# Performance work log

Hardware: AMD Instinct MI355X
Metric: run time of the kernel (lower is better)

The kernel has to match this reference:

```python
import jax, jax.numpy as jnp
import numpy as np


def setup_inputs() -> dict:
    key = jax.random.key(0)
    k1, k2, k3 = jax.random.split(key, 3)
    B, H, L, OUT = 4096, 2048, 8, 1024
    x = jax.random.normal(k1, (B, H), dtype=jnp.float32)
    W = jax.random.normal(k2, (L, H, H), dtype=jnp.float32)
    beta = jax.random.normal(k3, (H, OUT), dtype=jnp.float32)
    return {"x": x, "W": W, "beta": beta}


def _fcn_forward(x, W, beta):
    h = W.shape[-1]
    scale = 1.0 / jnp.sqrt(jnp.asarray(h, x.dtype))
    # Linear1d: (x[:,None]*W).sum(-1)/sqrt(h) == x @ W.T / sqrt(h); then ReLU.
    def layer(y, Wi):
        y = jax.nn.relu(jnp.einsum('bi,oi->bo', y, Wi) * scale)
        return y, None
    y, _ = jax.lax.scan(layer, x, W)
    # readout: y @ beta / h
    return jnp.einsum('bh,ho->bo', y, beta) / h


def reference(x, W, beta):
    return _fcn_forward(x, W, beta)
```

## Files before the change

kernel.cpp:

```cpp
#include <hip/hip_runtime.h>
#include <cstdint>
#include <cstddef>

typedef __bf16          bf16x8  __attribute__((ext_vector_type(8)));
typedef float           f32x4   __attribute__((ext_vector_type(4)));
typedef unsigned short  u16x8   __attribute__((ext_vector_type(8)));

__device__ __forceinline__ unsigned short f32_bf16_rne(float f) {
  union { float f; unsigned u; } v; v.f = f;
  unsigned u = v.u + 0x7FFFu + ((v.u >> 16) & 1u);
  return (unsigned short)(u >> 16);
}

__global__ void cvt_f32_bf16(const float* __restrict__ in,
                             unsigned short* __restrict__ out, int n8) {
  int idx = blockIdx.x * 256 + threadIdx.x;
  int stride = gridDim.x * 256;
  for (int i = idx; i < n8; i += stride) {
    float4 a = ((const float4*)in)[2 * (size_t)i];
    float4 b = ((const float4*)in)[2 * (size_t)i + 1];
    u16x8 o;
    o[0] = f32_bf16_rne(a.x); o[1] = f32_bf16_rne(a.y);
    o[2] = f32_bf16_rne(a.z); o[3] = f32_bf16_rne(a.w);
    o[4] = f32_bf16_rne(b.x); o[5] = f32_bf16_rne(b.y);
    o[6] = f32_bf16_rne(b.z); o[7] = f32_bf16_rne(b.w);
    *(u16x8*)(out + (size_t)i * 8) = o;
  }
}

__global__ void cvt_transpose(const float* __restrict__ in,
                              unsigned short* __restrict__ out, int H, int O) {
  __shared__ float tile[32][33];
  int o0 = blockIdx.x * 32, h0 = blockIdx.y * 32;
  int tx = threadIdx.x & 31, ty = threadIdx.x >> 5;
  #pragma unroll
  for (int i = ty; i < 32; i += 8)
    tile[i][tx] = in[(size_t)(h0 + i) * O + (o0 + tx)];
  __syncthreads();
  #pragma unroll
  for (int i = ty; i < 32; i += 8)
    out[(size_t)(o0 + i) * H + (h0 + tx)] = f32_bf16_rne(tile[tx][i]);
}

#define GLOAD(gp, lp)                                                   \
  __builtin_amdgcn_global_load_lds(                                     \
      (const __attribute__((address_space(1))) void*)(gp),              \
      (__attribute__((address_space(3))) void*)(lp), 16, 0, 0)

#define MFMA16 __builtin_amdgcn_mfma_f32_16x16x32_bf16


#define PHASE(KK, STAGE)                                                      \
  do {                                                                        \
    const int c = cc##KK;                                                     \
    bf16x8 a0 = *(const bf16x8*)(cA + aBase + 0 * 1024 + c);                  \
    bf16x8 a1 = *(const bf16x8*)(cA + aBase + 1 * 1024 + c);                  \
    bf16x8 a2 = *(const bf16x8*)(cA + aBase + 2 * 1024 + c);                  \
    bf16x8 a3 = *(const bf16x8*)(cA + aBase + 3 * 1024 + c);                  \
    bf16x8 b0 = *(const bf16x8*)(cB + bBase + 0 * 1024 + c);                  \
    bf16x8 b1 = *(const bf16x8*)(cB + bBase + 1 * 1024 + c);                  \
    bf16x8 b2 = *(const bf16x8*)(cB + bBase + 2 * 1024 + c);                  \
    bf16x8 b3 = *(const bf16x8*)(cB + bBase + 3 * 1024 + c);                  \
    STAGE                                                                     \
    __builtin_amdgcn_sched_barrier(0);                                        \
    __builtin_amdgcn_s_barrier();                                             \
    asm volatile("s_waitcnt lgkmcnt(0)" ::: "memory");                        \
    __builtin_amdgcn_sched_barrier(0);                                        \
    __builtin_amdgcn_s_setprio(1);                                            \
    acc[0][0] = MFMA16(a0, b0, acc[0][0], 0, 0, 0);                           \
    acc[0][1] = MFMA16(a0, b1, acc[0][1], 0, 0, 0);                           \
    acc[0][2] = MFMA16(a0, b2, acc[0][2], 0, 0, 0);                           \
    acc[0][3] = MFMA16(a0, b3, acc[0][3], 0, 0, 0);                           \
    acc[1][0] = MFMA16(a1, b0, acc[1][0], 0, 0, 0);                           \
    acc[1][1] = MFMA16(a1, b1, acc[1][1], 0, 0, 0);                           \
    acc[1][2] = MFMA16(a1, b2, acc[1][2], 0, 0, 0);                           \
    acc[1][3] = MFMA16(a1, b3, acc[1][3], 0, 0, 0);                           \
    acc[2][0] = MFMA16(a2, b0, acc[2][0], 0, 0, 0);                           \
    acc[2][1] = MFMA16(a2, b1, acc[2][1], 0, 0, 0);                           \
    acc[2][2] = MFMA16(a2, b2, acc[2][2], 0, 0, 0);                           \
    acc[2][3] = MFMA16(a2, b3, acc[2][3], 0, 0, 0);                           \
    acc[3][0] = MFMA16(a3, b0, acc[3][0], 0, 0, 0);                           \
    acc[3][1] = MFMA16(a3, b1, acc[3][1], 0, 0, 0);                           \
    acc[3][2] = MFMA16(a3, b2, acc[3][2], 0, 0, 0);                           \
    acc[3][3] = MFMA16(a3, b3, acc[3][3], 0, 0, 0);                           \
    __builtin_amdgcn_s_setprio(0);                                            \
    __builtin_amdgcn_sched_barrier(0);                                        \
    __builtin_amdgcn_s_barrier();                                             \
  } while (0)

__global__ __launch_bounds__(512, 2)
void gemm128x256(const unsigned short* __restrict__ A,
                 const unsigned short* __restrict__ B,
                 unsigned short* __restrict__ Cp, int N, int K, float scale) {
  __shared__ __bf16 As[3 * 128 * 64] __attribute__((aligned(16)));
  __shared__ __bf16 Bs[3 * 256 * 64] __attribute__((aligned(16)));

  const int tid  = threadIdx.x;
  const int lane = tid & 63;
  const int wave = tid >> 6;
  const int wr   = wave >> 2;
  const int wc   = wave & 3;
  const int l16  = lane & 15;
  const int kgrp = lane >> 4;

  const int brow0 = blockIdx.y * 128;
  const int bcol0 = blockIdx.x * 256;

  const int xorv  = (l16 & 7) << 3;
  const int cc0   = (kgrp * 8) ^ xorv;
  const int cc1   = (32 + kgrp * 8) ^ xorv;
  const int aBase = (wr * 64 + l16) * 64;
  const int bBase = (wc * 64 + l16) * 64;

  const int srow = tid >> 3;
  const int scol = ((tid & 7) * 8) ^ ((srow & 7) << 3);
  const unsigned short* gA0 = A + (size_t)(brow0 +   0 + srow) * K + scol;
  const unsigned short* gA1 = A + (size_t)(brow0 +  64 + srow) * K + scol;
  const unsigned short* gB0 = B + (size_t)(bcol0 +   0 + srow) * K + scol;
  const unsigned short* gB1 = B + (size_t)(bcol0 +  64 + srow) * K + scol;
  const unsigned short* gB2 = B + (size_t)(bcol0 + 128 + srow) * K + scol;
  const unsigned short* gB3 = B + (size_t)(bcol0 + 192 + srow) * K + scol;

  f32x4 acc[4][4] = {};

  const int NT = K >> 6;

  {
    GLOAD(gA0, &As[0 * 4096 + tid * 8]);
    GLOAD(gA1, &As[1 * 4096 + tid * 8]);
    GLOAD(gB0, &Bs[0 * 4096 + tid * 8]);
    GLOAD(gB1, &Bs[1 * 4096 + tid * 8]);
    GLOAD(gB2, &Bs[2 * 4096 + tid * 8]);
    GLOAD(gB3, &Bs[3 * 4096 + tid * 8]);
    GLOAD(gA0 + 64, &As[8192 + 0 * 4096 + tid * 8]);
    GLOAD(gA1 + 64, &As[8192 + 1 * 4096 + tid * 8]);
    GLOAD(gB0 + 64, &Bs[16384 + 0 * 4096 + tid * 8]);
    GLOAD(gB1 + 64, &Bs[16384 + 1 * 4096 + tid * 8]);
    GLOAD(gB2 + 64, &Bs[16384 + 2 * 4096 + tid * 8]);
    GLOAD(gB3 + 64, &Bs[16384 + 3 * 4096 + tid * 8]);
    asm volatile("s_waitcnt vmcnt(6)" ::: "memory");
    __builtin_amdgcn_s_barrier();
  }

  int s = 0;
  for (int t = 0; t < NT; ++t) {
    const __bf16* cA = &As[s * 8192];
    const __bf16* cB = &Bs[s * 16384];
    int su = s + 2; if (su >= 3) su -= 3;
    __bf16* dA = &As[su * 8192];
    __bf16* dB = &Bs[su * 16384];
    const bool stg = (t < NT - 2);
    const size_t ko = (size_t)(t + 2) * 64;

    PHASE(0,
      if (stg) {
        GLOAD(gA0 + ko, dA + 0 * 4096 + tid * 8);
        GLOAD(gA1 + ko, dA + 1 * 4096 + tid * 8);
        GLOAD(gB0 + ko, dB + 0 * 4096 + tid * 8);
      }
    );
    PHASE(1,
      if (stg) {
        GLOAD(gB1 + ko, dB + 1 * 4096 + tid * 8);
        GLOAD(gB2 + ko, dB + 2 * 4096 + tid * 8);
        GLOAD(gB3 + ko, dB + 3 * 4096 + tid * 8);
        asm volatile("s_waitcnt vmcnt(6)" ::: "memory");
      } else if (t == NT - 2) {
        asm volatile("s_waitcnt vmcnt(0)" ::: "memory");
      }
    );
    s = s + 1; if (s == 3) s = 0;
  }

  const int crow0 = brow0 + wr * 64 + kgrp * 4;
  const int ccol0 = bcol0 + wc * 64 + l16;
  #pragma unroll
  for (int m = 0; m < 4; ++m)
    #pragma unroll
    for (int n = 0; n < 4; ++n)
      #pragma unroll
      for (int j = 0; j < 4; ++j) {
        float v = acc[m][n][j] * scale;
        v = v > 0.0f ? v : 0.0f;
        Cp[(size_t)(crow0 + m * 16 + j) * N + (ccol0 + n * 16)] = f32_bf16_rne(v);
      }
}

__global__ __launch_bounds__(256)
void gemm_bt_f32(const unsigned short* __restrict__ A,
                 const unsigned short* __restrict__ B,
                 float* __restrict__ C, int N, int K, float scale) {
  __shared__ __bf16 As[128 * 32] __attribute__((aligned(16)));
  __shared__ __bf16 Bs[128 * 32] __attribute__((aligned(16)));

  const int tid  = threadIdx.x;
  const int lane = tid & 63;
  const int wave = tid >> 6;
  const int wr   = wave >> 1, wc = wave & 1;
  const int l16  = lane & 15, kgrp = lane >> 4;

  const int brow0 = blockIdx.y * 128;
  const int bcol0 = blockIdx.x * 128;

  const int offb  = wave * 2048 + lane * 16;
  const int srow  = offb >> 6;
  const int selem = (offb & 63) >> 1;
  const unsigned short* gA0 = A + (size_t)(brow0 + srow) * K + selem;
  const unsigned short* gA1 = A + (size_t)(brow0 + srow + 16) * K + selem;
  const unsigned short* gB0 = B + (size_t)(bcol0 + srow) * K + selem;
  const unsigned short* gB1 = B + (size_t)(bcol0 + srow + 16) * K + selem;
  __bf16* lA0 = &As[wave * 1024];
  __bf16* lA1 = &As[wave * 1024 + 512];
  __bf16* lB0 = &Bs[wave * 1024];
  __bf16* lB1 = &Bs[wave * 1024 + 512];

  f32x4 acc[4][4] = {};
  const int aoff = (wr * 64 + l16) * 32 + kgrp * 8;
  const int boff = (wc * 64 + l16) * 32 + kgrp * 8;

  for (int k0 = 0; k0 < K; k0 += 32) {
    GLOAD(gA0 + k0, lA0);
    GLOAD(gA1 + k0, lA1);
    GLOAD(gB0 + k0, lB0);
    GLOAD(gB1 + k0, lB1);
    asm volatile("s_waitcnt vmcnt(0)" ::: "memory");
    __syncthreads();

    bf16x8 af[4], bfv[4];
    #pragma unroll
    for (int m = 0; m < 4; ++m)
      af[m] = *(const bf16x8*)(As + aoff + m * 16 * 32);
    #pragma unroll
    for (int n = 0; n < 4; ++n)
      bfv[n] = *(const bf16x8*)(Bs + boff + n * 16 * 32);
    #pragma unroll
    for (int m = 0; m < 4; ++m)
      #pragma unroll
      for (int n = 0; n < 4; ++n)
        acc[m][n] = MFMA16(af[m], bfv[n], acc[m][n], 0, 0, 0);
    __syncthreads();
  }

  const int crow0 = brow0 + wr * 64 + kgrp * 4;
  const int ccol0 = bcol0 + wc * 64 + l16;
  #pragma unroll
  for (int m = 0; m < 4; ++m)
    #pragma unroll
    for (int n = 0; n < 4; ++n)
      #pragma unroll
      for (int j = 0; j < 4; ++j)
        C[(size_t)(crow0 + m * 16 + j) * N + (ccol0 + n * 16)] =
            acc[m][n][j] * scale;
}

extern "C" void kernel_launch(void* const* d_in, const int* in_sizes, int n_in,
                              void* d_out, int out_size, void* d_ws, size_t ws_size,
                              hipStream_t stream) {
  const float* x    = (const float*)d_in[0];
  const float* W    = (const float*)d_in[1];
  const float* beta = (const float*)d_in[2];
  float* out = (float*)d_out;

  const int Bn = 4096, H = 2048, L = 8, O = 1024;

  unsigned short* y0    = (unsigned short*)d_ws;
  unsigned short* y1    = y0 + (size_t)Bn * H;
  unsigned short* Wb    = y1 + (size_t)Bn * H;
  unsigned short* betaT = Wb + (size_t)H * H;

  {
    int n8 = Bn * H / 8;
    int grid = (n8 + 255) / 256;
    if (grid > 2048) grid = 2048;
    cvt_f32_bf16<<<grid, 256, 0, stream>>>(x, y0, n8);
  }
  cvt_transpose<<<dim3(O / 32, H / 32), 256, 0, stream>>>(beta, betaT, H, O);

  const float s1 = 0.02209708691207961f;
  unsigned short* yin = y0;
  unsigned short* yout = y1;
  for (int l = 0; l < L; ++l) {
    int n8 = H * H / 8;
    int grid = (n8 + 255) / 256;
    if (grid > 2048) grid = 2048;
    cvt_f32_bf16<<<grid, 256, 0, stream>>>(W + (size_t)l * H * H, Wb, n8);
    gemm128x256<<<dim3(H / 256, Bn / 128), 512, 0, stream>>>(yin, Wb, yout, H, H, s1);
    unsigned short* t = yin; yin = yout; yout = t;
  }
  gemm_bt_f32<<<dim3(O / 128, Bn / 128), 256, 0, stream>>>(yin, betaT, out, O, H,
                                                           1.0f / 2048.0f);
}
```

Baseline: 408.5 us.

## Software-pipeline LDS fragment reads in GEMM and batch weight conversion

The GEMM main loop now double-buffers register fragments: while MFMAs run on the current K-tile, the next tile's fragments are read from LDS, and there is one barrier per 64-wide K step instead of two. This is meant to hide LDS read latency behind matrix math, at the cost of doubled fragment register pressure under the 2-block occupancy bound. Separately, all eight layers' weights are converted to bf16 in a single launch before the layer loop, replacing eight per-layer conversion launches. This needs a workspace large enough for every layer's bf16 weights.

```diff
diff --git a/kernel.cpp b/kernel.cpp
--- a/kernel.cpp
+++ b/kernel.cpp
@@ -49,49 +49,69 @@
 
 #define MFMA16 __builtin_amdgcn_mfma_f32_16x16x32_bf16
 
-
-#define PHASE(KK, STAGE)                                                      \
-  do {                                                                        \
-    const int c = cc##KK;                                                     \
-    bf16x8 a0 = *(const bf16x8*)(cA + aBase + 0 * 1024 + c);                  \
-    bf16x8 a1 = *(const bf16x8*)(cA + aBase + 1 * 1024 + c);                  \
-    bf16x8 a2 = *(const bf16x8*)(cA + aBase + 2 * 1024 + c);                  \
-    bf16x8 a3 = *(const bf16x8*)(cA + aBase + 3 * 1024 + c);                  \
-    bf16x8 b0 = *(const bf16x8*)(cB + bBase + 0 * 1024 + c);                  \
-    bf16x8 b1 = *(const bf16x8*)(cB + bBase + 1 * 1024 + c);                  \
-    bf16x8 b2 = *(const bf16x8*)(cB + bBase + 2 * 1024 + c);                  \
-    bf16x8 b3 = *(const bf16x8*)(cB + bBase + 3 * 1024 + c);                  \
-    STAGE                                                                     \
-    __builtin_amdgcn_sched_barrier(0);                                        \
-    __builtin_amdgcn_s_barrier();                                             \
-    asm volatile("s_waitcnt lgkmcnt(0)" ::: "memory");                        \
-    __builtin_amdgcn_sched_barrier(0);                                        \
-    __builtin_amdgcn_s_setprio(1);                                            \
-    acc[0][0] = MFMA16(a0, b0, acc[0][0], 0, 0, 0);                           \
-    acc[0][1] = MFMA16(a0, b1, acc[0][1], 0, 0, 0);                           \
-    acc[0][2] = MFMA16(a0, b2, acc[0][2], 0, 0, 0);                           \
-    acc[0][3] = MFMA16(a0, b3, acc[0][3], 0, 0, 0);                           \
-    acc[1][0] = MFMA16(a1, b0, acc[1][0], 0, 0, 0);                           \
-    acc[1][1] = MFMA16(a1, b1, acc[1][1], 0, 0, 0);                           \
-    acc[1][2] = MFMA16(a1, b2, acc[1][2], 0, 0, 0);                           \
-    acc[1][3] = MFMA16(a1, b3, acc[1][3], 0, 0, 0);                           \
-    acc[2][0] = MFMA16(a2, b0, acc[2][0], 0, 0, 0);                           \
-    acc[2][1] = MFMA16(a2, b1, acc[2][1], 0, 0, 0);                           \
-    acc[2][2] = MFMA16(a2, b2, acc[2][2], 0, 0, 0);                           \
-    acc[2][3] = MFMA16(a2, b3, acc[2][3], 0, 0, 0);                           \
-    acc[3][0] = MFMA16(a3, b0, acc[3][0], 0, 0, 0);                           \
-    acc[3][1] = MFMA16(a3, b1, acc[3][1], 0, 0, 0);                           \
-    acc[3][2] = MFMA16(a3, b2, acc[3][2], 0, 0, 0);                           \
-    acc[3][3] = MFMA16(a3, b3, acc[3][3], 0, 0, 0);                           \
-    __builtin_amdgcn_s_setprio(0);                                            \
-    __builtin_amdgcn_sched_barrier(0);                                        \
-    __builtin_amdgcn_s_barrier();                                             \
+__device__ __forceinline__ void read_frags(bf16x8 (&fa)[2][4], bf16x8 (&fb)[2][4],
+                                           const __bf16* sa, const __bf16* sb,
+                                           int aBase, int bBase, int cc0, int cc1) {
+  #pragma unroll
+  for (int kk = 0; kk < 2; ++kk) {
+    const int c = kk ? cc1 : cc0;
+    #pragma unroll
+    for (int m = 0; m < 4; ++m)
+      fa[kk][m] = *(const bf16x8*)(sa + aBase + m * 1024 + c);
+    #pragma unroll
+    for (int n = 0; n < 4; ++n)
+      fb[kk][n] = *(const bf16x8*)(sb + bBase + n * 1024 + c);
+  }
+}
+
+__device__ __forceinline__ void mfma32(f32x4 (&acc)[4][4],
+                                       const bf16x8 (&fa)[2][4],
+                                       const bf16x8 (&fb)[2][4]) {
+  #pragma unroll
+  for (int kk = 0; kk < 2; ++kk)
+    #pragma unroll
+    for (int m = 0; m < 4; ++m)
+      #pragma unroll
+      for (int n = 0; n < 4; ++n)
+        acc[m][n] = MFMA16(fa[kk][m], fb[kk][n], acc[m][n], 0, 0, 0);
+}
+
+
+#define BODY(T, FA_C, FB_C, FA_N, FB_N)                                   \
+  do {                                                                    \
+    const int t_ = (T);                                                   \
+    if (t_ + 2 < NT) {                                                    \
+      const size_t ko = (size_t)(t_ + 2) * 64;                            \
+      __bf16* dA = As + sst * 8192;                                       \
+      __bf16* dB = Bs + sst * 16384;                                      \
+      GLOAD(gA0 + ko, dA + 0 * 4096 + tid * 8);                           \
+      GLOAD(gA1 + ko, dA + 1 * 4096 + tid * 8);                           \
+      GLOAD(gB0 + ko, dB + 0 * 4096 + tid * 8);                           \
+      GLOAD(gB1 + ko, dB + 1 * 4096 + tid * 8);                           \
+      GLOAD(gB2 + ko, dB + 2 * 4096 + tid * 8);                           \
+      GLOAD(gB3 + ko, dB + 3 * 4096 + tid * 8);                           \
+      asm volatile("s_waitcnt lgkmcnt(0)" ::: "memory");                  \
+      asm volatile("s_waitcnt vmcnt(6)" ::: "memory");                    \
+    } else {                                                              \
+      asm volatile("s_waitcnt lgkmcnt(0)" ::: "memory");                  \
+      asm volatile("s_waitcnt vmcnt(0)" ::: "memory");                    \
+    }                                                                     \
+    __builtin_amdgcn_s_barrier();                                         \
+    __builtin_amdgcn_sched_barrier(0);                                    \
+    if (t_ + 1 < NT)                                                      \
+      read_frags(FA_N, FB_N, As + srd * 8192, Bs + srd * 16384,           \
+                 aBase, bBase, cc0, cc1);                                 \
+    __builtin_amdgcn_s_setprio(1);                                        \
+    mfma32(acc, FA_C, FB_C);                                              \
+    __builtin_amdgcn_s_setprio(0);                                        \
+    sst = sst + 1; if (sst == 3) sst = 0;                                 \
+    srd = srd + 1; if (srd == 3) srd = 0;                                 \
   } while (0)
 
 __global__ __launch_bounds__(512, 2)
-void gemm128x256(const unsigned short* __restrict__ A,
-                 const unsigned short* __restrict__ B,
-                 unsigned short* __restrict__ Cp, int N, int K, float scale) {
+void gemm128x256p(const unsigned short* __restrict__ A,
+                  const unsigned short* __restrict__ B,
+                  unsigned short* __restrict__ Cp, int N, int K, float scale) {
   __shared__ __bf16 As[3 * 128 * 64] __attribute__((aligned(16)));
   __shared__ __bf16 Bs[3 * 256 * 64] __attribute__((aligned(16)));
 
@@ -121,7 +141,8 @@
   const unsigned short* gB2 = B + (size_t)(bcol0 + 128 + srow) * K + scol;
   const unsigned short* gB3 = B + (size_t)(bcol0 + 192 + srow) * K + scol;
 
-  f32x4 acc[4][4] = {};
+  f32x4  acc[4][4] = {};
+  bf16x8 fa0[2][4], fb0[2][4], fa1[2][4], fb1[2][4];
 
   const int NT = K >> 6;
 
@@ -140,36 +161,13 @@
     GLOAD(gB3 + 64, &Bs[16384 + 3 * 4096 + tid * 8]);
     asm volatile("s_waitcnt vmcnt(6)" ::: "memory");
     __builtin_amdgcn_s_barrier();
-  }
-
-  int s = 0;
-  for (int t = 0; t < NT; ++t) {
-    const __bf16* cA = &As[s * 8192];
-    const __bf16* cB = &Bs[s * 16384];
-    int su = s + 2; if (su >= 3) su -= 3;
-    __bf16* dA = &As[su * 8192];
-    __bf16* dB = &Bs[su * 16384];
-    const bool stg = (t < NT - 2);
-    const size_t ko = (size_t)(t + 2) * 64;
-
-    PHASE(0,
-      if (stg) {
-        GLOAD(gA0 + ko, dA + 0 * 4096 + tid * 8);
-        GLOAD(gA1 + ko, dA + 1 * 4096 + tid * 8);
-        GLOAD(gB0 + ko, dB + 0 * 4096 + tid * 8);
-      }
-    );
-    PHASE(1,
-      if (stg) {
-        GLOAD(gB1 + ko, dB + 1 * 4096 + tid * 8);
-        GLOAD(gB2 + ko, dB + 2 * 4096 + tid * 8);
-        GLOAD(gB3 + ko, dB + 3 * 4096 + tid * 8);
-        asm volatile("s_waitcnt vmcnt(6)" ::: "memory");
-      } else if (t == NT - 2) {
-        asm volatile("s_waitcnt vmcnt(0)" ::: "memory");
-      }
-    );
-    s = s + 1; if (s == 3) s = 0;
+    read_frags(fa0, fb0, As, Bs, aBase, bBase, cc0, cc1);
+  }
+
+  int sst = 2, srd = 1;
+  for (int t = 0; t < NT; t += 2) {
+    BODY(t,     fa0, fb0, fa1, fb1);
+    BODY(t + 1, fa1, fb1, fa0, fb0);
   }
 
   const int crow0 = brow0 + wr * 64 + kgrp * 4;
@@ -266,8 +264,12 @@
   unsigned short* y0    = (unsigned short*)d_ws;
   unsigned short* y1    = y0 + (size_t)Bn * H;
   unsigned short* Wb    = y1 + (size_t)Bn * H;
-  unsigned short* betaT = Wb + (size_t)H * H;
-
+  unsigned short* betaT = Wb + (size_t)L * H * H;
+
+  {
+    int n8 = L * H * H / 8;
+    cvt_f32_bf16<<<2048, 256, 0, stream>>>(W, Wb, n8);
+  }
   {
     int n8 = Bn * H / 8;
     int grid = (n8 + 255) / 256;
@@ -280,11 +282,8 @@
   unsigned short* yin = y0;
   unsigned short* yout = y1;
   for (int l = 0; l < L; ++l) {
-    int n8 = H * H / 8;
-    int grid = (n8 + 255) / 256;
-    if (grid > 2048) grid = 2048;
-    cvt_f32_bf16<<<grid, 256, 0, stream>>>(W + (size_t)l * H * H, Wb, n8);
-    gemm128x256<<<dim3(H / 256, Bn / 128), 512, 0, stream>>>(yin, Wb, yout, H, H, s1);
+    gemm128x256p<<<dim3(H / 256, Bn / 128), 512, 0, stream>>>(
+        yin, Wb + (size_t)l * H * H, yout, H, H, s1);
     unsigned short* t = yin; yin = yout; yout = t;
   }
   gemm_bt_f32<<<dim3(O / 128, Bn / 128), 256, 0, stream>>>(yin, betaT, out, O, H,
```

After: 404.6 us. Within noise of the previous version (-1.0%).
